# Kernel tuning notes

Hardware: AMD Instinct MI355X
Metric: run time of the kernel (lower is better)

The kernel has to match this reference:

```python
import jax, jax.numpy as jnp
import numpy as np
from jax import lax

VOL_RANGE = (-40.0, -40.0, -1.0, 40.0, 40.0, 5.4)
VOXEL_SIZE = 0.4
GRID_SHAPE = (200, 200, 16)  # int((hi-lo)/voxel_size) per axis
G = 1024                     # number of gaussians
C = 17                       # feature channels (semantic classes)
MAHA_THRESH = 7.5


def _make_grid_coords():
    # generate_grid(grid_shape, offset=0.5) * voxel_size + vol_range[:3]
    axes = [(jnp.arange(GRID_SHAPE[i], dtype=jnp.float32) + 0.5) * VOXEL_SIZE + VOL_RANGE[i]
            for i in range(3)]
    gx, gy, gz = jnp.meshgrid(*axes, indexing='ij')
    return jnp.stack([gx, gy, gz], axis=-1).reshape(-1, 3)  # [N, 3]


def _quat_to_rotmat(q):
    # q: [..., 4] (w, x, y, z), assumed normalized
    w, x, y, z = q[..., 0], q[..., 1], q[..., 2], q[..., 3]
    R = jnp.stack([
        1 - 2 * (y * y + z * z), 2 * (x * y - w * z), 2 * (x * z + w * y),
        2 * (x * y + w * z), 1 - 2 * (x * x + z * z), 2 * (y * z - w * x),
        2 * (x * z - w * y), 2 * (y * z + w * x), 1 - 2 * (x * x + y * y),
    ], axis=-1)
    return R.reshape(*q.shape[:-1], 3, 3)


def setup_inputs() -> dict:
    key = jax.random.key(0)
    k1, k2, k3, k4, k5 = jax.random.split(key, 5)
    lo = jnp.asarray(VOL_RANGE[:3], dtype=jnp.float32)
    hi = jnp.asarray(VOL_RANGE[3:], dtype=jnp.float32)
    means3d = lo + (hi - lo) * jax.random.uniform(k1, (1, G, 3), dtype=jnp.float32)
    opacities = jax.random.uniform(k2, (1, G, 1), dtype=jnp.float32)
    features = jax.random.normal(k3, (1, G, C), dtype=jnp.float32)
    # SPD covariances: R diag(s^2) R^T with realistic ~1m scales
    quats = jax.random.normal(k4, (1, G, 4), dtype=jnp.float32)
    quats = quats / jnp.linalg.norm(quats, axis=-1, keepdims=True)
    R = _quat_to_rotmat(quats)                                   # [1, G, 3, 3]
    scales = 0.5 + jax.random.uniform(k5, (1, G, 3), dtype=jnp.float32)  # in [0.5, 1.5] m
    covariances = jnp.einsum('bgij,bgj,bgkj->bgik', R, scales ** 2, R)
    return {
        'grid_coords': _make_grid_coords(),
        'means3d': means3d,
        'opacities': opacities,
        'features': features,
        'covariances': covariances,
    }


def _splat_one_batch(coords, means, ops, feats, covs):
    # coords: [N, 3]; means: [G, 3]; ops: [G]; feats: [G, C]; covs: [G, 3, 3]
    N = coords.shape[0]
    c = feats.shape[-1]
    inv_covs = jnp.linalg.inv(covs)  # [G, 3, 3]

    def step(carry, inp):
        dsum, fsum, cnt = carry
        mu, A, op, ft = inp
        diff = coords - mu                                  # [N, 3]
        maha = jnp.einsum('ni,ij,nj->n', diff, A, diff)     # [N]
        mask = maha <= MAHA_THRESH
        w = jnp.where(mask, op * jnp.exp(-0.5 * maha), 0.0)  # density contribution
        mf = mask.astype(coords.dtype)
        dsum = dsum + w
        fsum = fsum + mf[:, None] * (op * ft)[None, :]       # feature contribution
        cnt = cnt + mf
        return (dsum, fsum, cnt), None

    init = (jnp.zeros((N,), coords.dtype),
            jnp.zeros((N, c), coords.dtype),
            jnp.zeros((N,), coords.dtype))
    (dsum, fsum, cnt), _ = lax.scan(step, init, (means, inv_covs, ops, feats))
    # running-mean update in the torch loop == masked mean over gaussians
    denom = jnp.maximum(cnt, 1.0)
    return dsum / denom, fsum / denom[:, None]


def reference(grid_coords, means3d, opacities, features, covariances):
    dens, fts = jax.vmap(_splat_one_batch, in_axes=(None, 0, 0, 0, 0))(
        grid_coords, means3d, opacities[..., 0], features, covariances)
    B = means3d.shape[0]
    dens = dens.reshape(B, *GRID_SHAPE, 1)
    fts = fts.reshape(B, *GRID_SHAPE, features.shape[-1])
    return dens, fts
```

## Files before the change

### kernel.cpp

```cpp
#include <hip/hip_runtime.h>
#include <math.h>

#define G_N 1024
#define C_N 17
#define NX 200
#define NY 200
#define NZ 16
#define N_VOX (NX * NY * NZ)
#define MAHA_T 7.5f
#define CAP 64

__launch_bounds__(64, 4)
__global__ void gv_fused_kernel(const float* __restrict__ means,
                                const float* __restrict__ ops,
                                const float* __restrict__ feats,
                                const float* __restrict__ covs,
                                float* __restrict__ dens_out,
                                float* __restrict__ feat_out) {
    __shared__ unsigned short s_list[G_N];
    __shared__ __align__(16) float4 s_gd[CAP * 7];
    __shared__ __align__(16) float  s_out[64 * C_N];

    const int lane = threadIdx.x;
    const int bx = blockIdx.x, by = blockIdx.y;

    const float x0 = -40.f + (float)(bx * 4) * 0.4f;
    const float x1 = x0 + 1.6f;
    const float y0 = -40.f + (float)(by * 4) * 0.4f;
    const float y1 = y0 + 1.6f;

    int total = 0;
    for (int r = 0; r < 16; ++r) {
        int g = r * 64 + lane;
        float mx = means[3 * g], my = means[3 * g + 1], mz = means[3 * g + 2];
        float c00 = covs[9 * g], c11 = covs[9 * g + 4], c22 = covs[9 * g + 8];
        float hx = sqrtf(MAHA_T * c00) * 1.01f + 0.01f;
        float hy = sqrtf(MAHA_T * c11) * 1.01f + 0.01f;
        float hz = sqrtf(MAHA_T * c22) * 1.01f + 0.01f;
        bool hit = (mx - hx <= x1) && (mx + hx >= x0) &&
                   (my - hy <= y1) && (my + hy >= y0) &&
                   (mz - hz <= 5.4f) && (mz + hz >= -1.0f);
        unsigned long long m = __ballot(hit);
        int rank = __popcll(m & ((1ull << lane) - 1ull));
        if (hit) s_list[total + rank] = (unsigned short)g;
        total += __popcll(m);
    }

    const int z = lane & 15;
    const int yv = lane >> 4;
    const int X0 = bx * 4;
    const int Y = by * 4 + yv;

    float cx0, cx1, cx2, cx3, cy, cz;
    {
#pragma clang fp contract(off)
        cx0 = ((float)X0 + 0.5f) * 0.4f + -40.0f;
        cx1 = ((float)(X0 + 1) + 0.5f) * 0.4f + -40.0f;
        cx2 = ((float)(X0 + 2) + 0.5f) * 0.4f + -40.0f;
        cx3 = ((float)(X0 + 3) + 0.5f) * 0.4f + -40.0f;
        cy  = ((float)Y + 0.5f) * 0.4f + -40.0f;
        cz  = ((float)z + 0.5f) * 0.4f + -1.0f;
    }

    float dsa = 0.f, dsb = 0.f, dsc = 0.f, dsd = 0.f;
    float cna = 0.f, cnb = 0.f, cnc = 0.f, cnd = 0.f;
    float fa[C_N], fb[C_N], fc[C_N], fd[C_N];
#pragma unroll
    for (int c = 0; c < C_N; ++c) { fa[c] = 0.f; fb[c] = 0.f; fc[c] = 0.f; fd[c] = 0.f; }

#define ACC(F, DS, CN, MH) { DS = fmaf(q0.w, __expf(-0.5f * (MH)), DS); CN += 1.f; \
    F[0] += q2.z;  F[1] += q2.w;  F[2] += q3.x;  F[3] += q3.y;  F[4] += q3.z; \
    F[5] += q3.w;  F[6] += q4.x;  F[7] += q4.y;  F[8] += q4.z;  F[9] += q4.w; \
    F[10] += q5.x; F[11] += q5.y; F[12] += q5.z; F[13] += q5.w; F[14] += q6.x; \
    F[15] += q6.y; F[16] += q6.z; }

    for (int cb = 0; cb < total; cb += CAP) {
        const int nc = min(CAP, total - cb);
        __syncthreads();
        if (lane < nc) {
            int g = (int)s_list[cb + lane];
            const float* cv = covs + g * 9;
            double c00 = cv[0], c01 = cv[1], c02 = cv[2];
            double c11 = cv[4], c12 = cv[5], c22 = cv[8];
            double m00 = c11 * c22 - c12 * c12;
            double m01 = c02 * c12 - c01 * c22;
            double m02 = c01 * c12 - c02 * c11;
            double det = c00 * m00 + c01 * m01 + c02 * m02;
            double inv = 1.0 / det;
            float a00 = (float)(m00 * inv);
            float a01 = (float)(m01 * inv);
            float a02 = (float)(m02 * inv);
            float a11 = (float)((c00 * c22 - c02 * c02) * inv);
            float a12 = (float)((c02 * c01 - c00 * c12) * inv);
            float a22 = (float)((c00 * c11 - c01 * c01) * inv);
            float mx = means[3 * g], my = means[3 * g + 1], mz = means[3 * g + 2];
            float op = ops[g];
            const float* ft = feats + g * C_N;
            float4* o = s_gd + lane * 7;
            o[0] = make_float4(mx, my, mz, op);
            o[1] = make_float4(a00, a11, a22, 2.f * a01);
            o[2] = make_float4(2.f * a02, 2.f * a12, op * ft[0], op * ft[1]);
            o[3] = make_float4(op * ft[2], op * ft[3], op * ft[4], op * ft[5]);
            o[4] = make_float4(op * ft[6], op * ft[7], op * ft[8], op * ft[9]);
            o[5] = make_float4(op * ft[10], op * ft[11], op * ft[12], op * ft[13]);
            o[6] = make_float4(op * ft[14], op * ft[15], op * ft[16], 0.f);
        }
        __syncthreads();
        for (int j = 0; j < nc; ++j) {
            const float4* rowp = s_gd + j * 7;
            float4 q0 = rowp[0], q1 = rowp[1], q2 = rowp[2];
            float d0a = cx0 - q0.x, d0b = cx1 - q0.x;
            float d0c = cx2 - q0.x, d0d = cx3 - q0.x;
            float d1 = cy - q0.y, d2 = cz - q0.z;
            float s1 = q2.x * d2;
            float p  = fmaf(q1.w, d1, s1);
            float v  = fmaf(q1.y, d1, q2.y * d2);
            float w  = q1.z * d2;
            float t  = fmaf(d1, v, d2 * w);
            float ua = fmaf(q1.x, d0a, p);
            float ub = fmaf(q1.x, d0b, p);
            float uc = fmaf(q1.x, d0c, p);
            float ud = fmaf(q1.x, d0d, p);
            float mA = fmaf(d0a, ua, t);
            float mB = fmaf(d0b, ub, t);
            float mC = fmaf(d0c, uc, t);
            float mD = fmaf(d0d, ud, t);
            bool ha = mA <= MAHA_T, hb = mB <= MAHA_T;
            bool hc = mC <= MAHA_T, hd = mD <= MAHA_T;
            if (ha | hb | hc | hd) {
                float4 q3 = rowp[3], q4 = rowp[4], q5 = rowp[5], q6 = rowp[6];
                if (ha) ACC(fa, dsa, cna, mA);
                if (hb) ACC(fb, dsb, cnb, mB);
                if (hc) ACC(fc, dsc, cnc, mC);
                if (hd) ACC(fd, dsd, cnd, mD);
            }
        }
    }
    __syncthreads();

    const float4* lsrc = (const float4*)s_out;

#define EPI(F, DS, CN, XI) { \
    const float rd = 1.f / fmaxf(CN, 1.f); \
    const int nb = 16 * (4 * by + 200 * (X0 + (XI))); \
    dens_out[nb + lane] = DS * rd; \
    _Pragma("unroll") \
    for (int c = 0; c < C_N; ++c) s_out[lane * C_N + c] = F[c] * rd; \
    float4* gout = (float4*)(feat_out + (long)nb * C_N); \
    _Pragma("unroll") \
    for (int r = 0; r < 4; ++r) gout[lane + 64 * r] = lsrc[lane + 64 * r]; \
    if (lane < 16) gout[256 + lane] = lsrc[256 + lane]; \
    __syncthreads(); }

    EPI(fa, dsa, cna, 0);
    EPI(fb, dsb, cnb, 1);
    EPI(fc, dsc, cnc, 2);
    EPI(fd, dsd, cnd, 3);
}

extern "C" void kernel_launch(void* const* d_in, const int* in_sizes, int n_in,
                              void* d_out, int out_size, void* d_ws, size_t ws_size,
                              hipStream_t stream) {
    const float* means3d     = (const float*)d_in[1];
    const float* opacities   = (const float*)d_in[2];
    const float* features    = (const float*)d_in[3];
    const float* covariances = (const float*)d_in[4];

    float* dens_out = (float*)d_out;
    float* feat_out = (float*)d_out + N_VOX;

    dim3 grid(NX / 4, NY / 4);
    gv_fused_kernel<<<grid, 64, 0, stream>>>(means3d, opacities, features,
                                             covariances, dens_out, feat_out);
}
```

Baseline: 24.65 us.

## Precompute per-gaussian params in a prep kernel and use two-wave 8x4 column tiles

Adds a prep kernel that computes each gaussian's inverse covariance, opacity-scaled features and a packed culling box once, storing them in workspace. The splat kernel now culls from these compact float4 boxes and gathers the precomputed 8-float4 rows into shared memory cooperatively, so the double-precision inverse is not recomputed in every block. Blocks grow to two waves covering an 8x4 column footprint that share one gaussian list, and the epilogue uses per-wave staging without barriers. The trade-offs are an extra kernel launch with a dependency between the two kernels, a larger cull footprint per block that can admit more candidates per wave, and fewer blocks in the grid.

```diff
diff --git a/kernel.cpp b/kernel.cpp
--- a/kernel.cpp
+++ b/kernel.cpp
@@ -10,54 +10,99 @@
 #define MAHA_T 7.5f
 #define CAP 64
 
-__launch_bounds__(64, 4)
-__global__ void gv_fused_kernel(const float* __restrict__ means,
-                                const float* __restrict__ ops,
-                                const float* __restrict__ feats,
-                                const float* __restrict__ covs,
+__global__ void gv_prep_kernel(const float* __restrict__ means,
+                               const float* __restrict__ ops,
+                               const float* __restrict__ feats,
+                               const float* __restrict__ covs,
+                               float4* __restrict__ gp4,
+                               float4* __restrict__ cull4) {
+    int g = blockIdx.x * blockDim.x + threadIdx.x;
+    if (g >= G_N) return;
+    const float* cv = covs + g * 9;
+    double c00 = cv[0], c01 = cv[1], c02 = cv[2];
+    double c11 = cv[4], c12 = cv[5], c22 = cv[8];
+    double m00 = c11 * c22 - c12 * c12;
+    double m01 = c02 * c12 - c01 * c22;
+    double m02 = c01 * c12 - c02 * c11;
+    double det = c00 * m00 + c01 * m01 + c02 * m02;
+    double inv = 1.0 / det;
+    float a00 = (float)(m00 * inv);
+    float a01 = (float)(m01 * inv);
+    float a02 = (float)(m02 * inv);
+    float a11 = (float)((c00 * c22 - c02 * c02) * inv);
+    float a12 = (float)((c02 * c01 - c00 * c12) * inv);
+    float a22 = (float)((c00 * c11 - c01 * c01) * inv);
+    float mx = means[3 * g], my = means[3 * g + 1], mz = means[3 * g + 2];
+    float op = ops[g];
+    const float* ft = feats + g * C_N;
+    float4* o = gp4 + g * 8;
+    o[0] = make_float4(mx, my, mz, op);
+    o[1] = make_float4(a00, a11, a22, 2.f * a01);
+    o[2] = make_float4(2.f * a02, 2.f * a12, op * ft[0], op * ft[1]);
+    o[3] = make_float4(op * ft[2], op * ft[3], op * ft[4], op * ft[5]);
+    o[4] = make_float4(op * ft[6], op * ft[7], op * ft[8], op * ft[9]);
+    o[5] = make_float4(op * ft[10], op * ft[11], op * ft[12], op * ft[13]);
+    o[6] = make_float4(op * ft[14], op * ft[15], op * ft[16], 0.f);
+    float hx = sqrtf(MAHA_T * (float)c00) * 1.01f + 0.01f;
+    float hy = sqrtf(MAHA_T * (float)c11) * 1.01f + 0.01f;
+    float hz = sqrtf(MAHA_T * (float)c22) * 1.01f + 0.01f;
+    bool zok = (mz - hz <= 5.4f) && (mz + hz >= -1.0f);
+    cull4[g] = make_float4(zok ? (mx - hx) : 3.0e38f, mx + hx, my - hy, my + hy);
+}
+
+__launch_bounds__(128, 3)
+__global__ void gv_splat_kernel(const float4* __restrict__ gp4,
+                                const float4* __restrict__ cull4,
                                 float* __restrict__ dens_out,
                                 float* __restrict__ feat_out) {
     __shared__ unsigned short s_list[G_N];
-    __shared__ __align__(16) float4 s_gd[CAP * 7];
-    __shared__ __align__(16) float  s_out[64 * C_N];
-
-    const int lane = threadIdx.x;
+    __shared__ __align__(16) float4 s_gd[CAP * 8];
+    __shared__ __align__(16) float  s_out[2 * 64 * C_N];
+    __shared__ int s_wcnt[2];
+
+    const int tid = threadIdx.x;
+    const int wave = tid >> 6;
+    const int lane = tid & 63;
     const int bx = blockIdx.x, by = blockIdx.y;
 
-    const float x0 = -40.f + (float)(bx * 4) * 0.4f;
-    const float x1 = x0 + 1.6f;
+    const float x0 = -40.f + (float)(bx * 8) * 0.4f;
+    const float x1 = x0 + 3.2f;
     const float y0 = -40.f + (float)(by * 4) * 0.4f;
     const float y1 = y0 + 1.6f;
 
-    int total = 0;
-    for (int r = 0; r < 16; ++r) {
-        int g = r * 64 + lane;
-        float mx = means[3 * g], my = means[3 * g + 1], mz = means[3 * g + 2];
-        float c00 = covs[9 * g], c11 = covs[9 * g + 4], c22 = covs[9 * g + 8];
-        float hx = sqrtf(MAHA_T * c00) * 1.01f + 0.01f;
-        float hy = sqrtf(MAHA_T * c11) * 1.01f + 0.01f;
-        float hz = sqrtf(MAHA_T * c22) * 1.01f + 0.01f;
-        bool hit = (mx - hx <= x1) && (mx + hx >= x0) &&
-                   (my - hy <= y1) && (my + hy >= y0) &&
-                   (mz - hz <= 5.4f) && (mz + hz >= -1.0f);
+    unsigned short* s_stage = (unsigned short*)s_gd;
+    int base = 0;
+#pragma unroll
+    for (int r = 0; r < 8; ++r) {
+        int g = wave * 512 + r * 64 + lane;
+        float4 cb = cull4[g];
+        bool hit = (cb.x <= x1) && (cb.y >= x0) && (cb.z <= y1) && (cb.w >= y0);
         unsigned long long m = __ballot(hit);
         int rank = __popcll(m & ((1ull << lane) - 1ull));
-        if (hit) s_list[total + rank] = (unsigned short)g;
-        total += __popcll(m);
+        if (hit) s_stage[wave * 512 + base + rank] = (unsigned short)g;
+        base += __popcll(m);
     }
+    if (lane == 0) s_wcnt[wave] = base;
+    __syncthreads();
+    const int c0 = s_wcnt[0];
+    const int total = c0 + s_wcnt[1];
+    const int off = wave ? c0 : 0;
+    for (int i = lane; i < base; i += 64)
+        s_list[off + i] = s_stage[wave * 512 + i];
+    __syncthreads();
 
     const int z = lane & 15;
     const int yv = lane >> 4;
-    const int X0 = bx * 4;
+    const int Xb = bx * 8 + 4 * wave;
     const int Y = by * 4 + yv;
 
     float cx0, cx1, cx2, cx3, cy, cz;
     {
 #pragma clang fp contract(off)
-        cx0 = ((float)X0 + 0.5f) * 0.4f + -40.0f;
-        cx1 = ((float)(X0 + 1) + 0.5f) * 0.4f + -40.0f;
-        cx2 = ((float)(X0 + 2) + 0.5f) * 0.4f + -40.0f;
-        cx3 = ((float)(X0 + 3) + 0.5f) * 0.4f + -40.0f;
+        cx0 = ((float)Xb + 0.5f) * 0.4f + -40.0f;
+        cx1 = ((float)(Xb + 1) + 0.5f) * 0.4f + -40.0f;
+        cx2 = ((float)(Xb + 2) + 0.5f) * 0.4f + -40.0f;
+        cx3 = ((float)(Xb + 3) + 0.5f) * 0.4f + -40.0f;
         cy  = ((float)Y + 0.5f) * 0.4f + -40.0f;
         cz  = ((float)z + 0.5f) * 0.4f + -1.0f;
     }
@@ -77,37 +122,14 @@
     for (int cb = 0; cb < total; cb += CAP) {
         const int nc = min(CAP, total - cb);
         __syncthreads();
-        if (lane < nc) {
-            int g = (int)s_list[cb + lane];
-            const float* cv = covs + g * 9;
-            double c00 = cv[0], c01 = cv[1], c02 = cv[2];
-            double c11 = cv[4], c12 = cv[5], c22 = cv[8];
-            double m00 = c11 * c22 - c12 * c12;
-            double m01 = c02 * c12 - c01 * c22;
-            double m02 = c01 * c12 - c02 * c11;
-            double det = c00 * m00 + c01 * m01 + c02 * m02;
-            double inv = 1.0 / det;
-            float a00 = (float)(m00 * inv);
-            float a01 = (float)(m01 * inv);
-            float a02 = (float)(m02 * inv);
-            float a11 = (float)((c00 * c22 - c02 * c02) * inv);
-            float a12 = (float)((c02 * c01 - c00 * c12) * inv);
-            float a22 = (float)((c00 * c11 - c01 * c01) * inv);
-            float mx = means[3 * g], my = means[3 * g + 1], mz = means[3 * g + 2];
-            float op = ops[g];
-            const float* ft = feats + g * C_N;
-            float4* o = s_gd + lane * 7;
-            o[0] = make_float4(mx, my, mz, op);
-            o[1] = make_float4(a00, a11, a22, 2.f * a01);
-            o[2] = make_float4(2.f * a02, 2.f * a12, op * ft[0], op * ft[1]);
-            o[3] = make_float4(op * ft[2], op * ft[3], op * ft[4], op * ft[5]);
-            o[4] = make_float4(op * ft[6], op * ft[7], op * ft[8], op * ft[9]);
-            o[5] = make_float4(op * ft[10], op * ft[11], op * ft[12], op * ft[13]);
-            o[6] = make_float4(op * ft[14], op * ft[15], op * ft[16], 0.f);
+        for (int k = tid; k < nc * 8; k += 128) {
+            int row = k >> 3, sub = k & 7;
+            int g = (int)s_list[cb + row];
+            s_gd[k] = gp4[g * 8 + sub];
         }
         __syncthreads();
         for (int j = 0; j < nc; ++j) {
-            const float4* rowp = s_gd + j * 7;
+            const float4* rowp = s_gd + j * 8;
             float4 q0 = rowp[0], q1 = rowp[1], q2 = rowp[2];
             float d0a = cx0 - q0.x, d0b = cx1 - q0.x;
             float d0c = cx2 - q0.x, d0d = cx3 - q0.x;
@@ -136,21 +158,20 @@
             }
         }
     }
-    __syncthreads();
-
-    const float4* lsrc = (const float4*)s_out;
+
+    float* fw = s_out + wave * (64 * C_N);
+    const float4* lsrc = (const float4*)fw;
 
 #define EPI(F, DS, CN, XI) { \
     const float rd = 1.f / fmaxf(CN, 1.f); \
-    const int nb = 16 * (4 * by + 200 * (X0 + (XI))); \
+    const int nb = 16 * (4 * by + 200 * (Xb + (XI))); \
     dens_out[nb + lane] = DS * rd; \
     _Pragma("unroll") \
-    for (int c = 0; c < C_N; ++c) s_out[lane * C_N + c] = F[c] * rd; \
+    for (int c = 0; c < C_N; ++c) fw[lane * C_N + c] = F[c] * rd; \
     float4* gout = (float4*)(feat_out + (long)nb * C_N); \
     _Pragma("unroll") \
     for (int r = 0; r < 4; ++r) gout[lane + 64 * r] = lsrc[lane + 64 * r]; \
-    if (lane < 16) gout[256 + lane] = lsrc[256 + lane]; \
-    __syncthreads(); }
+    if (lane < 16) gout[256 + lane] = lsrc[256 + lane]; }
 
     EPI(fa, dsa, cna, 0);
     EPI(fb, dsb, cnb, 1);
@@ -168,8 +189,12 @@
 
     float* dens_out = (float*)d_out;
     float* feat_out = (float*)d_out + N_VOX;
-
-    dim3 grid(NX / 4, NY / 4);
-    gv_fused_kernel<<<grid, 64, 0, stream>>>(means3d, opacities, features,
-                                             covariances, dens_out, feat_out);
+    float4* gp4   = (float4*)d_ws;
+    float4* cull4 = (float4*)((char*)d_ws + G_N * 128);
+
+    gv_prep_kernel<<<(G_N + 255) / 256, 256, 0, stream>>>(means3d, opacities,
+                                                          features, covariances,
+                                                          gp4, cull4);
+    dim3 grid(NX / 8, NY / 4);
+    gv_splat_kernel<<<grid, 128, 0, stream>>>(gp4, cull4, dens_out, feat_out);
 }
```

Measured after the change: 26.50 us. +7.5%, slower.
